# Kernel tuning notes

Hardware: AMD Instinct MI355X
Metric: run time of the kernel (lower is better)

The kernel has to match this reference:

```python
import jax, jax.numpy as jnp
import numpy as np

B, NPG, K, DIN, DOUT, EMB, HEADS = 64, 1024, 32, 512, 512, 32, 4
HD = EMB // HEADS  # head dim = 8


def layernorm(x, g, b, eps=1e-5):
    m = jnp.mean(x, axis=-1, keepdims=True)
    v = jnp.var(x, axis=-1, keepdims=True)
    return (x - m) / jnp.sqrt(v + eps) * g + b


def _xavier(key, out_f, in_f, gain=0.5):
    std = gain * np.sqrt(2.0 / (in_f + out_f))
    return jax.random.normal(key, (out_f, in_f), dtype=jnp.float32) * std


def setup_inputs() -> dict:
    key = jax.random.key(0)
    ks = jax.random.split(key, 16)
    N = B * NPG
    x = jax.random.normal(ks[0], (N, DIN), dtype=jnp.float32)
    # roughly orthonormal-column scale for eigenvectors
    eigenvectors = jax.random.normal(ks[1], (N, K), dtype=jnp.float32) / np.sqrt(NPG)
    eigenvalues = jax.random.uniform(ks[2], (B * K,), dtype=jnp.float32) * 2.0
    eig_mask = jnp.ones((B * K,), dtype=bool)
    batch = jnp.repeat(jnp.arange(B, dtype=jnp.int64), NPG)
    z = jnp.zeros
    o = jnp.ones
    return {
        "x": x, "eigenvectors": eigenvectors, "eigenvalues": eigenvalues,
        "eig_mask": eig_mask, "batch": batch,
        "W1": _xavier(ks[3], 32, 1), "b1": z(32), "g1": o(32), "be1": z(32),
        "W2": _xavier(ks[4], 32, 32), "b2": z(32), "g2": o(32), "be2": z(32),
        "Wqkv": _xavier(ks[5], 3 * EMB, EMB), "bqkv": z(3 * EMB),
        "Wo": _xavier(ks[6], EMB, EMB), "bo": z(EMB),
        "Wf1": _xavier(ks[7], 64, 32), "bf1": z(64),
        "Wf2": _xavier(ks[8], 1, 64), "bf2": z(1),
        "Wp": _xavier(ks[9], DOUT, DIN), "bp": z(DOUT),
        "gp": o(DOUT), "bep": z(DOUT),
    }


def reference(x, eigenvectors, eigenvalues, eig_mask, batch,
              W1, b1, g1, be1, W2, b2, g2, be2,
              Wqkv, bqkv, Wo, bo, Wf1, bf1, Wf2, bf2, Wp, bp, gp, bep):
    # ---- eigenvalue set encoder (batched over all graphs at once) ----
    ev = eigenvalues.reshape(B, K, 1)                       # [B,K,1]
    h = ev @ W1.T + b1                                      # [B,K,32]
    h = jax.nn.relu(layernorm(h, g1, be1))
    h = layernorm(h @ W2.T + b2, g2, be2)                   # [B,K,32]
    # ---- multi-head self-attention over the K eigenvalues ----
    padding = ~eig_mask.reshape(B, K)                       # True = masked out
    qkv = h @ Wqkv.T + bqkv                                 # [B,K,96]
    q, k_, v = jnp.split(qkv, 3, axis=-1)
    def heads(t):
        return t.reshape(B, K, HEADS, HD).transpose(0, 2, 1, 3)  # [B,H,K,hd]
    q, k_, v = heads(q), heads(k_), heads(v)
    scores = jnp.einsum('bhqd,bhkd->bhqk', q, k_) / np.sqrt(HD)
    scores = jnp.where(padding[:, None, None, :], -1e9, scores)
    attn = jax.nn.softmax(scores, axis=-1)
    ctx = jnp.einsum('bhqk,bhkd->bhqd', attn, v)
    ctx = ctx.transpose(0, 2, 1, 3).reshape(B, K, EMB)
    ctx = ctx @ Wo.T + bo                                   # [B,K,32]
    # ---- filter generator ----
    f = jnp.tanh(jax.nn.relu(ctx @ Wf1.T + bf1) @ Wf2.T + bf2)[..., 0]  # [B,K]
    filters = jnp.where(padding, 0.0, f)
    # ---- spectral filtering per graph (equal-size graphs -> reshape) ----
    xg = x.reshape(B, NPG, DIN)
    vg = eigenvectors.reshape(B, NPG, K)
    x_freq = jnp.einsum('bnk,bnd->bkd', vg, xg)             # U^T x
    x_spat = jnp.einsum('bnk,bkd->bnd', vg, filters[:, :, None] * x_freq)
    out = layernorm(x_spat @ Wp.T + bp, gp, bep)            # [B,NPG,DOUT]
    return out.reshape(B * NPG, DOUT)
```

## Files before the change

kernel.cpp:

```cpp
#include <hip/hip_runtime.h>
#include <math.h>

#define B    64
#define NPG  1024
#define KEIG 32
#define DIN  512
#define DOUT 512
#define NPART 8

typedef float  f32x4  __attribute__((ext_vector_type(4)));
typedef short  bf16x8 __attribute__((ext_vector_type(8)));

__device__ __forceinline__ unsigned short f2bf(float x) {
    union { float f; unsigned int u; } v; v.f = x;
    unsigned int r = v.u + 0x7FFFu + ((v.u >> 16) & 1u);
    return (unsigned short)(r >> 16);
}

__device__ __forceinline__ float rsum32(float v) {
    v += __shfl_xor(v, 1, 32);
    v += __shfl_xor(v, 2, 32);
    v += __shfl_xor(v, 4, 32);
    v += __shfl_xor(v, 8, 32);
    v += __shfl_xor(v, 16, 32);
    return v;
}
__device__ __forceinline__ float rmax32(float v) {
    v = fmaxf(v, __shfl_xor(v, 1, 32));
    v = fmaxf(v, __shfl_xor(v, 2, 32));
    v = fmaxf(v, __shfl_xor(v, 4, 32));
    v = fmaxf(v, __shfl_xor(v, 8, 32));
    v = fmaxf(v, __shfl_xor(v, 16, 32));
    return v;
}

__global__ __launch_bounds__(1024) void k1_filters(
    const float* __restrict__ eigenvalues,
    const float* __restrict__ W1,  const float* __restrict__ b1,
    const float* __restrict__ g1,  const float* __restrict__ be1,
    const float* __restrict__ W2,  const float* __restrict__ b2,
    const float* __restrict__ g2,  const float* __restrict__ be2,
    const float* __restrict__ Wqkv,const float* __restrict__ bqkv,
    const float* __restrict__ Wo,  const float* __restrict__ bo,
    const float* __restrict__ Wf1, const float* __restrict__ bf1,
    const float* __restrict__ Wf2, const float* __restrict__ bf2,
    float* __restrict__ filters)
{
    __shared__ float wts[224][33];
    __shared__ float hA[KEIG][33];
    __shared__ float hB[KEIG][33];
    __shared__ float qkv[KEIG][97];
    __shared__ float attn[4 * 1064];

    const int t = threadIdx.x;
    const int k = t >> 5;
    const int j = t & 31;
    const int b = blockIdx.x;

    {
        const int row = t >> 5, i = t & 31;
        wts[row][i]       = W2[t];
        wts[32 + row][i]  = Wqkv[t];
        wts[64 + row][i]  = Wqkv[1024 + t];
        wts[96 + row][i]  = Wqkv[2048 + t];
        wts[128 + row][i] = Wo[t];
        wts[160 + row][i] = Wf1[t];
        wts[192 + row][i] = Wf1[1024 + t];
    }

    const float ev = eigenvalues[b * KEIG + k];
    float h1 = ev * W1[j] + b1[j];
    {
        float m = rsum32(h1) * (1.f / 32.f);
        float d = h1 - m;
        float q = rsum32(d * d);
        float r = rsqrtf(q * (1.f / 32.f) + 1e-5f);
        h1 = fmaxf(d * r * g1[j] + be1[j], 0.f);
    }
    hA[k][j] = h1;
    __syncthreads();

    {
        float a = b2[j];
        #pragma unroll
        for (int i = 0; i < 32; ++i) a += hA[k][i] * wts[j][i];
        float m = rsum32(a) * (1.f / 32.f);
        float d = a - m;
        float q = rsum32(d * d);
        float r = rsqrtf(q * (1.f / 32.f) + 1e-5f);
        hB[k][j] = d * r * g2[j] + be2[j];
    }
    __syncthreads();

    {
        float aq = bqkv[j], ak = bqkv[32 + j], av = bqkv[64 + j];
        #pragma unroll
        for (int i = 0; i < 32; ++i) {
            float hv = hB[k][i];
            aq += hv * wts[32 + j][i];
            ak += hv * wts[64 + j][i];
            av += hv * wts[96 + j][i];
        }
        qkv[k][j]      = aq;
        qkv[k][32 + j] = ak;
        qkv[k][64 + j] = av;
    }
    __syncthreads();

    {
        const float inv = 0.35355339059327373f;
        float sc[4];
        #pragma unroll
        for (int hh = 0; hh < 4; ++hh) {
            float s = 0.f;
            #pragma unroll
            for (int d2 = 0; d2 < 8; ++d2)
                s += qkv[k][hh * 8 + d2] * qkv[j][32 + hh * 8 + d2];
            sc[hh] = s * inv;
        }
        #pragma unroll
        for (int hh = 0; hh < 4; ++hh) {
            float mx  = rmax32(sc[hh]);
            float e   = __expf(sc[hh] - mx);
            float den = rsum32(e);
            attn[hh * 1064 + k * 33 + j] = e / den;
        }
    }
    __syncthreads();

    {
        const int hh = j >> 3;
        float c = 0.f;
        #pragma unroll
        for (int k2 = 0; k2 < 32; ++k2)
            c += attn[hh * 1064 + k * 33 + k2] * qkv[k2][64 + j];
        hA[k][j] = c;
    }
    __syncthreads();

    {
        float o = bo[j];
        #pragma unroll
        for (int i = 0; i < 32; ++i) o += hA[k][i] * wts[128 + j][i];
        hB[k][j] = o;
    }
    __syncthreads();

    {
        float r0 = bf1[j], r1 = bf1[32 + j];
        #pragma unroll
        for (int i = 0; i < 32; ++i) {
            float ov = hB[k][i];
            r0 += ov * wts[160 + j][i];
            r1 += ov * wts[192 + j][i];
        }
        float fp = fmaxf(r0, 0.f) * Wf2[j] + fmaxf(r1, 0.f) * Wf2[32 + j];
        fp = rsum32(fp);
        if (j == 0) filters[b * KEIG + k] = tanhf(fp + bf2[0]);
    }
}

__global__ __launch_bounds__(256) void k2_xfreq_partial(
    const float* __restrict__ x, const float* __restrict__ eigvec,
    float* __restrict__ xfp)
{
    __shared__ float vtile[128][32];
    const int t  = threadIdx.x;
    const int b  = blockIdx.x >> 4;
    const int nc = (blockIdx.x >> 1) & 7;
    const int dh = blockIdx.x & 1;
    const int kq = t >> 6;
    const int ds = t & 63;
    const int d  = dh * 256 + ds * 4;
    const int n0 = nc * 128;

    const float* vb = eigvec + ((size_t)(b * NPG + n0)) * KEIG;
    #pragma unroll
    for (int e = 0; e < 16; ++e) {
        int idx = t + e * 256;
        ((float*)vtile)[idx] = vb[idx];
    }
    __syncthreads();

    float4 acc[8];
    #pragma unroll
    for (int i = 0; i < 8; ++i) acc[i] = make_float4(0.f, 0.f, 0.f, 0.f);

    const float* xb = x + ((size_t)(b * NPG + n0)) * DIN + d;
    #pragma unroll 4
    for (int n = 0; n < 128; ++n) {
        float4 xv = *(const float4*)(xb + (size_t)n * DIN);
        const float4* vp = (const float4*)&vtile[n][kq * 8];
        float4 v0 = vp[0], v1 = vp[1];
        acc[0].x += v0.x * xv.x; acc[0].y += v0.x * xv.y; acc[0].z += v0.x * xv.z; acc[0].w += v0.x * xv.w;
        acc[1].x += v0.y * xv.x; acc[1].y += v0.y * xv.y; acc[1].z += v0.y * xv.z; acc[1].w += v0.y * xv.w;
        acc[2].x += v0.z * xv.x; acc[2].y += v0.z * xv.y; acc[2].z += v0.z * xv.z; acc[2].w += v0.z * xv.w;
        acc[3].x += v0.w * xv.x; acc[3].y += v0.w * xv.y; acc[3].z += v0.w * xv.z; acc[3].w += v0.w * xv.w;
        acc[4].x += v1.x * xv.x; acc[4].y += v1.x * xv.y; acc[4].z += v1.x * xv.z; acc[4].w += v1.x * xv.w;
        acc[5].x += v1.y * xv.x; acc[5].y += v1.y * xv.y; acc[5].z += v1.y * xv.z; acc[5].w += v1.y * xv.w;
        acc[6].x += v1.z * xv.x; acc[6].y += v1.z * xv.y; acc[6].z += v1.z * xv.z; acc[6].w += v1.z * xv.w;
        acc[7].x += v1.w * xv.x; acc[7].y += v1.w * xv.y; acc[7].z += v1.w * xv.z; acc[7].w += v1.w * xv.w;
    }

    #pragma unroll
    for (int kk = 0; kk < 8; ++kk) {
        int kg = kq * 8 + kk;
        *(float4*)(xfp + (((size_t)nc * B + b) * KEIG + kg) * DIN + d) = acc[kk];
    }
}

__global__ __launch_bounds__(256) void k2b_combine(
    const float* __restrict__ xfp, const float* __restrict__ filters,
    float* __restrict__ F)
{
    const int t = threadIdx.x;
    const int m = blockIdx.x * 2 + (t >> 7);
    const int dp = (t & 127) * 4;

    const float* base = xfp + (size_t)m * DIN + dp;
    float4 s = *(const float4*)base;
    #pragma unroll
    for (int q = 1; q < NPART; ++q) {
        float4 sq = *(const float4*)(base + (size_t)q * (B * KEIG * DIN));
        s.x += sq.x; s.y += sq.y; s.z += sq.z; s.w += sq.w;
    }
    const float f = filters[m];
    float4 o = make_float4(s.x * f, s.y * f, s.z * f, s.w * f);
    *(float4*)(F + (size_t)m * DIN + dp) = o;
}

__global__ __launch_bounds__(256) void k3_G(
    const float* __restrict__ F, const float* __restrict__ Wp,
    unsigned short* __restrict__ Gt)
{
    __shared__ float a_lds[64][65];
    __shared__ float b_lds[64][65];

    const int t   = threadIdx.x;
    const int mt  = blockIdx.x >> 3;
    const int ot  = blockIdx.x & 7;
    const int m0  = mt * 64;
    const int o0  = ot * 64;
    const int tr  = t >> 4;
    const int tc  = t & 15;
    const int col4 = tc * 4;

    float acc[4][4] = {{0.f}};

    for (int d0 = 0; d0 < DIN; d0 += 64) {
        __syncthreads();
        #pragma unroll
        for (int p = 0; p < 4; ++p) {
            int r = p * 16 + tr;
            float4 s = *(const float4*)(F + (size_t)(m0 + r) * DIN + d0 + col4);
            a_lds[r][col4 + 0] = s.x;
            a_lds[r][col4 + 1] = s.y;
            a_lds[r][col4 + 2] = s.z;
            a_lds[r][col4 + 3] = s.w;
        }
        #pragma unroll
        for (int p = 0; p < 4; ++p) {
            int r = p * 16 + tr;
            float4 w = *(const float4*)(Wp + (size_t)(o0 + r) * DIN + d0 + col4);
            b_lds[r][col4 + 0] = w.x;
            b_lds[r][col4 + 1] = w.y;
            b_lds[r][col4 + 2] = w.z;
            b_lds[r][col4 + 3] = w.w;
        }
        __syncthreads();
        #pragma unroll 4
        for (int dd = 0; dd < 64; ++dd) {
            float a0 = a_lds[tr * 4 + 0][dd];
            float a1 = a_lds[tr * 4 + 1][dd];
            float a2 = a_lds[tr * 4 + 2][dd];
            float a3 = a_lds[tr * 4 + 3][dd];
            float b0 = b_lds[tc * 4 + 0][dd];
            float b1 = b_lds[tc * 4 + 1][dd];
            float b2 = b_lds[tc * 4 + 2][dd];
            float b3 = b_lds[tc * 4 + 3][dd];
            acc[0][0] += a0 * b0; acc[0][1] += a0 * b1; acc[0][2] += a0 * b2; acc[0][3] += a0 * b3;
            acc[1][0] += a1 * b0; acc[1][1] += a1 * b1; acc[1][2] += a1 * b2; acc[1][3] += a1 * b3;
            acc[2][0] += a2 * b0; acc[2][1] += a2 * b1; acc[2][2] += a2 * b2; acc[2][3] += a2 * b3;
            acc[3][0] += a3 * b0; acc[3][1] += a3 * b1; acc[3][2] += a3 * b2; acc[3][3] += a3 * b3;
        }
    }
    #pragma unroll
    for (int i = 0; i < 4; ++i) {
        int m  = m0 + tr * 4 + i;
        int bb = m >> 5, kk = m & 31;
        #pragma unroll
        for (int j = 0; j < 4; ++j) {
            int o = o0 + tc * 4 + j;
            Gt[((size_t)bb * DOUT + o) * KEIG + kk] = f2bf(acc[i][j]);
        }
    }
}

__global__ __launch_bounds__(256, 1) void k4_out(
    const float* __restrict__ eigvec, const unsigned short* __restrict__ Gt,
    const float* __restrict__ bp, const float* __restrict__ gp,
    const float* __restrict__ bep, float* __restrict__ out)
{
    __shared__ unsigned short gt_lds[512][40];
    __shared__ float prm[3 * 512];

    const int t  = threadIdx.x;
    const int b  = blockIdx.x >> 4;
    const int n0 = (blockIdx.x & 15) * 64;

    {
        const unsigned short* src = Gt + (size_t)b * (DOUT * KEIG);
        #pragma unroll
        for (int e = 0; e < 8; ++e) {
            int c = t + e * 256;
            int row = c >> 2, part = c & 3;
            bf16x8 v = *(const bf16x8*)(src + c * 8);
            *(bf16x8*)&gt_lds[row][part * 8] = v;
        }
    }
    #pragma unroll
    for (int e = 0; e < 6; ++e) {
        int idx = t + e * 256;
        prm[idx] = (idx < 512) ? bp[idx]
                 : (idx < 1024) ? gp[idx - 512] : bep[idx - 1024];
    }
    __syncthreads();

    const int w  = t >> 6;
    const int l  = t & 63;
    const int cl = l & 15;
    const int g  = l >> 4;
    const int kb = g * 8;

    bf16x8 afrag;
    {
        const float* ar = eigvec + ((size_t)(b * NPG + n0 + w * 16 + cl)) * KEIG + kb;
        float4 a0 = *(const float4*)(ar);
        float4 a1 = *(const float4*)(ar + 4);
        afrag[0] = (short)f2bf(a0.x); afrag[1] = (short)f2bf(a0.y);
        afrag[2] = (short)f2bf(a0.z); afrag[3] = (short)f2bf(a0.w);
        afrag[4] = (short)f2bf(a1.x); afrag[5] = (short)f2bf(a1.y);
        afrag[6] = (short)f2bf(a1.z); afrag[7] = (short)f2bf(a1.w);
    }

    f32x4 acc[32];
    #pragma unroll
    for (int ct = 0; ct < 32; ++ct) acc[ct] = (f32x4){0.f, 0.f, 0.f, 0.f};

    #pragma unroll
    for (int ct = 0; ct < 32; ++ct) {
        bf16x8 bfrag = *(const bf16x8*)&gt_lds[ct * 16 + cl][kb];
        acc[ct] = __builtin_amdgcn_mfma_f32_16x16x32_bf16(afrag, bfrag, acc[ct], 0, 0, 0);
    }

    float s[4] = {0.f, 0.f, 0.f, 0.f}, q[4] = {0.f, 0.f, 0.f, 0.f};
    #pragma unroll
    for (int ct = 0; ct < 32; ++ct) {
        float bpc = prm[ct * 16 + cl];
        #pragma unroll
        for (int j = 0; j < 4; ++j) {
            float v = acc[ct][j] + bpc;
            s[j] += v; q[j] += v * v;
        }
    }
    #pragma unroll
    for (int off = 1; off < 16; off <<= 1) {
        #pragma unroll
        for (int j = 0; j < 4; ++j) {
            s[j] += __shfl_xor(s[j], off, 16);
            q[j] += __shfl_xor(q[j], off, 16);
        }
    }
    float mh[4], rs[4];
    #pragma unroll
    for (int j = 0; j < 4; ++j) {
        mh[j] = s[j] * (1.f / 512.f);
        rs[j] = rsqrtf(q[j] * (1.f / 512.f) - mh[j] * mh[j] + 1e-5f);
    }

    const size_t rowbase = (size_t)b * NPG + n0 + w * 16 + g * 4;
    #pragma unroll
    for (int ct = 0; ct < 32; ++ct) {
        int col = ct * 16 + cl;
        float bpc = prm[col];
        float gpc = prm[512 + col];
        float bec = prm[1024 + col];
        #pragma unroll
        for (int j = 0; j < 4; ++j) {
            float v = (acc[ct][j] + bpc - mh[j]) * rs[j] * gpc + bec;
            __builtin_nontemporal_store(v, out + (rowbase + j) * DOUT + col);
        }
    }
}

extern "C" void kernel_launch(void* const* d_in, const int* in_sizes, int n_in,
                              void* d_out, int out_size, void* d_ws, size_t ws_size,
                              hipStream_t stream) {
    (void)in_sizes; (void)n_in; (void)out_size; (void)ws_size;
    const float* x    = (const float*)d_in[0];
    const float* vg   = (const float*)d_in[1];
    const float* ev   = (const float*)d_in[2];
    const float* W1   = (const float*)d_in[5];
    const float* b1   = (const float*)d_in[6];
    const float* g1   = (const float*)d_in[7];
    const float* be1  = (const float*)d_in[8];
    const float* W2   = (const float*)d_in[9];
    const float* b2   = (const float*)d_in[10];
    const float* g2   = (const float*)d_in[11];
    const float* be2  = (const float*)d_in[12];
    const float* Wqkv = (const float*)d_in[13];
    const float* bqkv = (const float*)d_in[14];
    const float* Wo   = (const float*)d_in[15];
    const float* bo   = (const float*)d_in[16];
    const float* Wf1  = (const float*)d_in[17];
    const float* bf1  = (const float*)d_in[18];
    const float* Wf2  = (const float*)d_in[19];
    const float* bf2  = (const float*)d_in[20];
    const float* Wp   = (const float*)d_in[21];
    const float* bp   = (const float*)d_in[22];
    const float* gp   = (const float*)d_in[23];
    const float* bep  = (const float*)d_in[24];

    float* outf    = (float*)d_out;
    float* ws      = (float*)d_ws;
    float* filters = ws;
    unsigned short* Gt = (unsigned short*)(ws + 4096);
    float* xfp     = outf;
    float* F       = outf + 16777216;

    hipLaunchKernelGGL(k1_filters, dim3(B), dim3(1024), 0, stream,
                       ev, W1, b1, g1, be1, W2, b2, g2, be2,
                       Wqkv, bqkv, Wo, bo, Wf1, bf1, Wf2, bf2, filters);
    hipLaunchKernelGGL(k2_xfreq_partial, dim3(B * 16), dim3(256), 0, stream,
                       x, vg, xfp);
    hipLaunchKernelGGL(k2b_combine, dim3(1024), dim3(256), 0, stream,
                       xfp, filters, F);
    hipLaunchKernelGGL(k3_G, dim3(32 * 8), dim3(256), 0, stream,
                       F, Wp, Gt);
    hipLaunchKernelGGL(k4_out, dim3(B * 16), dim3(256), 0, stream,
                       vg, Gt, bp, gp, bep, outf);
}
```

Measured before the change: 131.7 us.

## Run k4_out as single-wave blocks reading Gt and params from global memory

The output kernel now launches 4096 one-wave blocks instead of 1024 four-wave blocks. It drops the LDS staging of the per-graph Gt tile and of the bias/gamma/beta parameters along with the block barrier, and reads them straight from global memory (L2/L1 cached). The aim is to remove the LDS fill and sync overhead and to let more waves sit on each CU now that the 1-block launch bound is gone. The cost is that each wave refetches the 32KB Gt tile and the parameters from cache, adding global load traffic and latency.

```diff
diff --git a/kernel.cpp b/kernel.cpp
--- a/kernel.cpp
+++ b/kernel.cpp
@@ -296,45 +296,23 @@
     }
 }
 
-__global__ __launch_bounds__(256, 1) void k4_out(
+__global__ __launch_bounds__(64) void k4_out(
     const float* __restrict__ eigvec, const unsigned short* __restrict__ Gt,
     const float* __restrict__ bp, const float* __restrict__ gp,
     const float* __restrict__ bep, float* __restrict__ out)
 {
-    __shared__ unsigned short gt_lds[512][40];
-    __shared__ float prm[3 * 512];
-
-    const int t  = threadIdx.x;
-    const int b  = blockIdx.x >> 4;
-    const int n0 = (blockIdx.x & 15) * 64;
-
-    {
-        const unsigned short* src = Gt + (size_t)b * (DOUT * KEIG);
-        #pragma unroll
-        for (int e = 0; e < 8; ++e) {
-            int c = t + e * 256;
-            int row = c >> 2, part = c & 3;
-            bf16x8 v = *(const bf16x8*)(src + c * 8);
-            *(bf16x8*)&gt_lds[row][part * 8] = v;
-        }
-    }
-    #pragma unroll
-    for (int e = 0; e < 6; ++e) {
-        int idx = t + e * 256;
-        prm[idx] = (idx < 512) ? bp[idx]
-                 : (idx < 1024) ? gp[idx - 512] : bep[idx - 1024];
-    }
-    __syncthreads();
-
-    const int w  = t >> 6;
-    const int l  = t & 63;
+    const int wave = blockIdx.x;
+    const int b    = wave >> 6;
+    const int n0   = (wave & 63) * 16;
+
+    const int l  = threadIdx.x;
     const int cl = l & 15;
     const int g  = l >> 4;
     const int kb = g * 8;
 
     bf16x8 afrag;
     {
-        const float* ar = eigvec + ((size_t)(b * NPG + n0 + w * 16 + cl)) * KEIG + kb;
+        const float* ar = eigvec + ((size_t)(b * NPG + n0 + cl)) * KEIG + kb;
         float4 a0 = *(const float4*)(ar);
         float4 a1 = *(const float4*)(ar + 4);
         afrag[0] = (short)f2bf(a0.x); afrag[1] = (short)f2bf(a0.y);
@@ -343,20 +321,21 @@
         afrag[6] = (short)f2bf(a1.z); afrag[7] = (short)f2bf(a1.w);
     }
 
+    const unsigned short* gb = Gt + (size_t)b * (DOUT * KEIG);
     f32x4 acc[32];
     #pragma unroll
     for (int ct = 0; ct < 32; ++ct) acc[ct] = (f32x4){0.f, 0.f, 0.f, 0.f};
 
     #pragma unroll
     for (int ct = 0; ct < 32; ++ct) {
-        bf16x8 bfrag = *(const bf16x8*)&gt_lds[ct * 16 + cl][kb];
+        bf16x8 bfrag = *(const bf16x8*)(gb + (size_t)(ct * 16 + cl) * KEIG + kb);
         acc[ct] = __builtin_amdgcn_mfma_f32_16x16x32_bf16(afrag, bfrag, acc[ct], 0, 0, 0);
     }
 
     float s[4] = {0.f, 0.f, 0.f, 0.f}, q[4] = {0.f, 0.f, 0.f, 0.f};
     #pragma unroll
     for (int ct = 0; ct < 32; ++ct) {
-        float bpc = prm[ct * 16 + cl];
+        float bpc = bp[ct * 16 + cl];
         #pragma unroll
         for (int j = 0; j < 4; ++j) {
             float v = acc[ct][j] + bpc;
@@ -378,13 +357,13 @@
         rs[j] = rsqrtf(q[j] * (1.f / 512.f) - mh[j] * mh[j] + 1e-5f);
     }
 
-    const size_t rowbase = (size_t)b * NPG + n0 + w * 16 + g * 4;
+    const size_t rowbase = (size_t)b * NPG + n0 + g * 4;
     #pragma unroll
     for (int ct = 0; ct < 32; ++ct) {
         int col = ct * 16 + cl;
-        float bpc = prm[col];
-        float gpc = prm[512 + col];
-        float bec = prm[1024 + col];
+        float bpc = bp[col];
+        float gpc = gp[col];
+        float bec = bep[col];
         #pragma unroll
         for (int j = 0; j < 4; ++j) {
             float v = (acc[ct][j] + bpc - mh[j]) * rs[j] * gpc + bec;
@@ -437,6 +416,6 @@
                        xfp, filters, F);
     hipLaunchKernelGGL(k3_G, dim3(32 * 8), dim3(256), 0, stream,
                        F, Wp, Gt);
-    hipLaunchKernelGGL(k4_out, dim3(B * 16), dim3(256), 0, stream,
+    hipLaunchKernelGGL(k4_out, dim3(B * 64), dim3(64), 0, stream,
                        vg, Gt, bp, gp, bep, outf);
 }
```

After: 129.7 us. No clear change (-1.5%).
